# Performance work log

Hardware: AMD Instinct MI355X
Metric: run time of the kernel (lower is better)

## Reference

```python
import jax, jax.numpy as jnp
from jax import lax
import numpy as np

TOP_K = 2
CAPACITY_FACTOR = 1.0


def setup_inputs() -> dict:
    key = jax.random.key(0)
    kx, kg, k1, k2 = jax.random.split(key, 4)
    B, S, D, F, E = 8, 4096, 512, 1024, 16
    x = jax.random.normal(kx, (B, S, D), dtype=jnp.float32)
    w_gate = jax.random.normal(kg, (D, E), dtype=jnp.float32) * 0.02
    w1 = jax.random.normal(k1, (E, D, 2 * F), dtype=jnp.float32) * 0.02
    w2 = jax.random.normal(k2, (E, F, D), dtype=jnp.float32) * 0.02
    return {"x": x, "w_gate": w_gate, "w1": w1, "w2": w2}


def reference(x, w_gate, w1, w2):
    # Inference mode: no gating noise, dropout is identity.
    B, S, D = x.shape
    E = w_gate.shape[1]
    T = B * S
    capacity = max(1, int(CAPACITY_FACTOR * T / E))  # static

    flat = x.reshape(T, D)
    gate_logits = flat @ w_gate                      # [T, E]
    gate_scores = jax.nn.softmax(gate_logits, axis=-1)
    topk_vals, topk_idx = lax.top_k(gate_scores, TOP_K)  # [T, k]

    phi_mean = gate_scores.mean(axis=0)
    aux_loss = E * jnp.sum(phi_mean * phi_mean)

    # Per-expert combine weight for every token: [E, T]
    onehot = topk_idx[None, :, :] == jnp.arange(E)[:, None, None]  # [E, T, k]
    w_et = jnp.sum(jnp.where(onehot, topk_vals[None], 0.0), axis=-1)  # [E, T]

    # Capacity truncation: keep the `capacity` highest-weight tokens per expert
    sel_w, sel_idx = lax.top_k(w_et, capacity)  # [E, C]; unrouted picks have weight 0

    xs = flat[sel_idx]                                  # [E, C, D] gather
    h = jnp.einsum('ecd,edf->ecf', xs, w1)              # [E, C, 2F]
    h1, h2 = jnp.split(h, 2, axis=-1)
    act = h1 * jax.nn.silu(h2)                          # SwiGLU
    out_e = jnp.einsum('ecf,efd->ecd', act, w2) * sel_w[..., None]  # [E, C, D]

    combined = jnp.zeros((T, D), dtype=flat.dtype).at[sel_idx.reshape(-1)].add(
        out_e.reshape(-1, D))
    return combined.reshape(B, S, D), aux_loss
```

## Files before the change

kernel.cpp:

```cpp
#include <hip/hip_runtime.h>
#include <hip/hip_bf16.h>
#include <math.h>

#define T_TOK 32768
#define D_DIM 512
#define E_EXP 16
#define F_DIM 1024
#define C_CAP 2048

typedef __attribute__((ext_vector_type(8))) __bf16 bf16x8;
typedef __attribute__((ext_vector_type(4))) float f32x4;

__device__ __forceinline__ unsigned short f2bf(float f) {
  unsigned u = __float_as_uint(f);
  u += 0x7FFFu + ((u >> 16) & 1u);
  return (unsigned short)(u >> 16);
}

__device__ __forceinline__ void gld16(const void* gptr, void* ldsptr) {
  __builtin_amdgcn_global_load_lds(
      (__attribute__((address_space(1))) void*)(void*)gptr,
      (__attribute__((address_space(3))) void*)ldsptr, 16, 0, 0);
}

__global__ void transpose_conv_kernel(const float* __restrict__ in,
                                      unsigned short* __restrict__ out,
                                      int R, int Cc) {
  __shared__ float tile[32][33];
  int e = blockIdx.z;
  int r0 = blockIdx.y * 32, c0 = blockIdx.x * 32;
  const float* pin = in + (size_t)e * R * Cc;
  unsigned short* pout = out + (size_t)e * R * Cc;
  int tx = threadIdx.x, ty = threadIdx.y;
  #pragma unroll
  for (int i = 0; i < 32; i += 8)
    tile[ty + i][tx] = pin[(size_t)(r0 + ty + i) * Cc + c0 + tx];
  __syncthreads();
  #pragma unroll
  for (int i = 0; i < 32; i += 8)
    pout[(size_t)(c0 + ty + i) * R + r0 + tx] = f2bf(tile[tx][ty + i]);
}

__global__ __launch_bounds__(256) void gate_kernel(
    const float* __restrict__ x, const float* __restrict__ wg,
    float* __restrict__ w_et, float* __restrict__ phi_sum,
    unsigned short* __restrict__ xb) {
  __shared__ float wgl[D_DIM * E_EXP];
  __shared__ float phil[E_EXP];
  int tid = threadIdx.x;
  for (int i = tid; i < D_DIM * E_EXP; i += 256) wgl[i] = wg[i];
  if (tid < E_EXP) phil[tid] = 0.f;
  __syncthreads();

  int g = tid >> 4;
  int e = tid & 15;
  int t = blockIdx.x * 16 + g;

  float acc = 0.f;
  const float* xr = x + (size_t)t * D_DIM;
  #pragma unroll 4
  for (int d = 0; d < D_DIM; d += 4) {
    float4 xv = *(const float4*)(xr + d);
    acc = fmaf(xv.x, wgl[(d + 0) * 16 + e], acc);
    acc = fmaf(xv.y, wgl[(d + 1) * 16 + e], acc);
    acc = fmaf(xv.z, wgl[(d + 2) * 16 + e], acc);
    acc = fmaf(xv.w, wgl[(d + 3) * 16 + e], acc);
  }

  unsigned short* xrow = xb + (size_t)t * D_DIM;
  #pragma unroll
  for (int j = 0; j < 8; ++j) {
    int idx = j * 16 + e;
    float4 v = *(const float4*)(xr + idx * 4);
    ushort4 o;
    o.x = f2bf(v.x); o.y = f2bf(v.y); o.z = f2bf(v.z); o.w = f2bf(v.w);
    ((ushort4*)xrow)[idx] = o;
  }

  float m = acc;
  for (int off = 8; off; off >>= 1) m = fmaxf(m, __shfl_xor(m, off));
  float p = expf(acc - m);
  float s = p;
  for (int off = 8; off; off >>= 1) s += __shfl_xor(s, off);
  float score = p / s;
  atomicAdd(&phil[e], score);

  float v1 = score; int i1 = e;
  for (int off = 8; off; off >>= 1) {
    float ov = __shfl_xor(v1, off); int oi = __shfl_xor(i1, off);
    if (ov > v1 || (ov == v1 && oi < i1)) { v1 = ov; i1 = oi; }
  }
  float sc2 = (e == i1) ? -1.f : score;
  float v2 = sc2; int i2 = e;
  for (int off = 8; off; off >>= 1) {
    float ov = __shfl_xor(v2, off); int oi = __shfl_xor(i2, off);
    if (ov > v2 || (ov == v2 && oi < i2)) { v2 = ov; i2 = oi; }
  }
  if (e == 0) {
    w_et[(size_t)i1 * T_TOK + t] = v1;
    w_et[(size_t)i2 * T_TOK + t] = v2;
  }
  __syncthreads();
  if (tid < E_EXP) atomicAdd(&phi_sum[tid], phil[tid]);
}

__global__ void aux_kernel(const float* __restrict__ phi_sum, float* __restrict__ out_aux) {
  if (threadIdx.x == 0) {
    float s = 0.f;
    for (int e = 0; e < E_EXP; ++e) {
      float pm = phi_sum[e] / (float)T_TOK;
      s += pm * pm;
    }
    *out_aux = (float)E_EXP * s;
  }
}

template<int P>
__global__ __launch_bounds__(256) void s_hist(
    const float* __restrict__ w_et, unsigned* __restrict__ hist,
    const unsigned* __restrict__ prefix, const unsigned* __restrict__ done) {
  int c = blockIdx.x, e = blockIdx.y, tid = threadIdx.x;
  if (P > 0 && done[e]) return;
  __shared__ unsigned lh[2048];
  for (int i = tid; i < 2048; i += 256) lh[i] = 0;
  __syncthreads();
  const float* w = w_et + (size_t)e * T_TOK + c * 2048;
  unsigned pfx = (P > 0) ? prefix[e] : 0u;
  #pragma unroll
  for (int i = 0; i < 8; ++i) {
    unsigned b = __float_as_uint(w[i * 256 + tid]);
    if (P == 0) { if (b) atomicAdd(&lh[b >> 21], 1u); }
    else if (P == 1) { if ((b >> 21) == (pfx >> 21)) atomicAdd(&lh[(b >> 10) & 0x7FFu], 1u); }
    else { if ((b >> 10) == (pfx >> 10)) atomicAdd(&lh[b & 0x3FFu], 1u); }
  }
  __syncthreads();
  for (int i = tid; i < 2048; i += 256)
    if (lh[i]) atomicAdd(&hist[e * 2048 + i], lh[i]);
}

template<int P>
__global__ __launch_bounds__(1024) void s_pick(
    const unsigned* __restrict__ hist, unsigned* __restrict__ prefix,
    unsigned* __restrict__ krem, unsigned* __restrict__ done) {
  int tid = threadIdx.x, lane = tid & 63, e = tid >> 6;
  if (P > 0 && done[e]) return;
  const int BPL = (P == 2) ? 16 : 32;
  const int SH = (P == 0) ? 21 : (P == 1) ? 10 : 0;
  const unsigned* h = hist + e * 2048;
  unsigned S = 0;
  for (int i = 0; i < BPL; ++i) S += h[lane * BPL + i];
  unsigned U = S;
  #pragma unroll
  for (int off = 1; off < 64; off <<= 1) {
    unsigned t = __shfl_down(U, off);
    if (lane + off < 64) U += t;
  }
  unsigned Unext = __shfl_down(U, 1);
  if (lane == 63) Unext = 0;
  unsigned k = (P == 0) ? (unsigned)C_CAP : krem[e];
  if (P == 0 && lane == 0) {
    if (U < k) { done[e] = 1; prefix[e] = 0; krem[e] = 0; }
    else done[e] = 0;
  }
  if (U >= k && Unext < k) {
    unsigned cum = Unext; int chosen = 0; unsigned knew = 0;
    for (int i = BPL - 1; i >= 0; --i) {
      unsigned hh = h[lane * BPL + i];
      if (cum + hh >= k) { chosen = lane * BPL + i; knew = k - cum; break; }
      cum += hh;
    }
    if (P == 0) prefix[e] = ((unsigned)chosen) << SH;
    else prefix[e] = prefix[e] | (((unsigned)chosen) << SH);
    krem[e] = knew;
  }
}

__global__ __launch_bounds__(256) void s_count(
    const float* __restrict__ w_et, const unsigned* __restrict__ prefix,
    unsigned* __restrict__ cnt) {
  int c = blockIdx.x, e = blockIdx.y, tid = threadIdx.x;
  unsigned thr = prefix[e];
  const uint4* up = (const uint4*)(w_et + (size_t)e * T_TOK + c * 2048 + tid * 8);
  uint4 va = up[0], vb = up[1];
  unsigned gt = 0, eq = 0;
  unsigned vals[8] = {va.x, va.y, va.z, va.w, vb.x, vb.y, vb.z, vb.w};
  #pragma unroll
  for (int i = 0; i < 8; ++i) {
    if (vals[i] > thr) gt++;
    else if (vals[i] == thr) eq++;
  }
  __shared__ unsigned sc[256];
  sc[tid] = (gt << 16) | eq;
  __syncthreads();
  for (int s = 128; s; s >>= 1) {
    if (tid < s) sc[tid] += sc[tid + s];
    __syncthreads();
  }
  if (tid == 0) cnt[e * 16 + c] = sc[0];
}

__global__ __launch_bounds__(256) void s_write(
    const float* __restrict__ w_et, const unsigned* __restrict__ prefix,
    const unsigned* __restrict__ cnt,
    int* __restrict__ sel_idx, float* __restrict__ sel_w) {
  int c = blockIdx.x, e = blockIdx.y, tid = threadIdx.x;
  unsigned thr = prefix[e];
  __shared__ unsigned s_gb, s_eb, s_gt, s_eq;
  if (tid == 0) {
    unsigned g = 0, q = 0, gb = 0, eb = 0;
    #pragma unroll
    for (int c2 = 0; c2 < 16; ++c2) {
      unsigned p = cnt[e * 16 + c2];
      if (c2 < c) { gb += p >> 16; eb += p & 0xFFFFu; }
      g += p >> 16; q += p & 0xFFFFu;
    }
    s_gb = gb; s_eb = eb; s_gt = g; s_eq = (unsigned)C_CAP - g;
  }
  const uint4* up = (const uint4*)(w_et + (size_t)e * T_TOK + c * 2048 + tid * 8);
  uint4 va = up[0], vb = up[1];
  unsigned vals[8] = {va.x, va.y, va.z, va.w, vb.x, vb.y, vb.z, vb.w};
  unsigned gt = 0, eq = 0;
  #pragma unroll
  for (int i = 0; i < 8; ++i) {
    if (vals[i] > thr) gt++;
    else if (vals[i] == thr) eq++;
  }
  __shared__ unsigned sc[256];
  unsigned mine = (gt << 16) | eq;
  sc[tid] = mine;
  __syncthreads();
  for (int off = 1; off < 256; off <<= 1) {
    unsigned add = (tid >= off) ? sc[tid - off] : 0u;
    __syncthreads();
    sc[tid] += add;
    __syncthreads();
  }
  unsigned excl = sc[tid] - mine;
  unsigned gpos = s_gb + (excl >> 16);
  unsigned qpos = s_eb + (excl & 0xFFFFu);
  unsigned gtotal = s_gt, eqtake = s_eq;
  int* si = sel_idx + (size_t)e * C_CAP;
  float* sw = sel_w + (size_t)e * C_CAP;
  int tokbase = c * 2048 + tid * 8;
  #pragma unroll
  for (int i = 0; i < 8; ++i) {
    unsigned b = vals[i];
    if (b > thr) {
      si[gpos] = tokbase + i; sw[gpos] = __uint_as_float(b); gpos++;
    } else if (b == thr && qpos < eqtake) {
      si[gtotal + qpos] = tokbase + i; sw[gtotal + qpos] = __uint_as_float(b); qpos++;
    }
  }
}


#define PIPE_BARRIER() do { __builtin_amdgcn_s_barrier(); __builtin_amdgcn_sched_barrier(0); } while (0)

__global__ __launch_bounds__(256, 2) void gemm1_kernel(
    const unsigned short* __restrict__ xb,
    const unsigned short* __restrict__ w1t,
    const int* __restrict__ sel_idx,
    unsigned short* __restrict__ act) {
  __shared__ __align__(16) unsigned short As[5 * 4096];
  __shared__ __align__(16) unsigned short Bs[5 * 4096];
  int bid = (blockIdx.x & 7) * 512 + (blockIdx.x >> 3);
  int nt = bid & 15, mt = (bid >> 4) & 15, e = bid >> 8;
  int tid = threadIdx.x, lane = tid & 63, wid = tid >> 6;
  int wr = wid >> 1, wc = wid & 1;
  int cl = lane & 15, rg = lane >> 4;

  int c0 = tid, c1 = 256 + tid;
  int r0 = c0 >> 2, gk0 = (c0 & 3) ^ ((r0 >> 1) & 3);
  int r1 = c1 >> 2, gk1 = (c1 & 3) ^ ((r1 >> 1) & 3);
  int tok0 = sel_idx[e * C_CAP + mt * 128 + r0];
  int tok1 = sel_idx[e * C_CAP + mt * 128 + r1];
  const unsigned short* ag0 = xb + (size_t)tok0 * D_DIM + gk0 * 8;
  const unsigned short* ag1 = xb + (size_t)tok1 * D_DIM + gk1 * 8;
  int hcol0 = (r0 < 64) ? (nt * 64 + r0) : (F_DIM + nt * 64 + (r0 - 64));
  int hcol1 = (r1 < 64) ? (nt * 64 + r1) : (F_DIM + nt * 64 + (r1 - 64));
  const unsigned short* bg0 = w1t + ((size_t)e * 2 * F_DIM + hcol0) * D_DIM + gk0 * 8;
  const unsigned short* bg1 = w1t + ((size_t)e * 2 * F_DIM + hcol1) * D_DIM + gk1 * 8;
  char* Ab = (char*)As;
  char* Bb = (char*)Bs;

#define G1_STAGE(buf, kt) do { \
    gld16(ag0 + (kt) * 32, Ab + (buf) * 8192 + tid * 16); \
    gld16(ag1 + (kt) * 32, Ab + (buf) * 8192 + 4096 + tid * 16); \
    gld16(bg0 + (kt) * 32, Bb + (buf) * 8192 + tid * 16); \
    gld16(bg1 + (kt) * 32, Bb + (buf) * 8192 + 4096 + tid * 16); \
  } while (0)

  f32x4 zero = {0.f, 0.f, 0.f, 0.f};
  f32x4 acc[4][4];
  #pragma unroll
  for (int m = 0; m < 4; ++m)
    #pragma unroll
    for (int n = 0; n < 4; ++n) acc[m][n] = zero;

#define G1_COMPUTE(buf) do { \
    const unsigned short* Ap = As + (buf) * 4096; \
    const unsigned short* Bp = Bs + (buf) * 4096; \
    bf16x8 av[4], bv[4]; \
    _Pragma("unroll") \
    for (int m = 0; m < 4; ++m) { \
      int ra = wr * 64 + m * 16 + cl; \
      av[m] = *(const bf16x8*)&Ap[(ra * 4 + (rg ^ ((ra >> 1) & 3))) * 8]; \
    } \
    _Pragma("unroll") \
    for (int n = 0; n < 4; ++n) { \
      int rb = ((n < 2) ? (wc * 32 + n * 16) : (64 + wc * 32 + (n - 2) * 16)) + cl; \
      bv[n] = *(const bf16x8*)&Bp[(rb * 4 + (rg ^ ((rb >> 1) & 3))) * 8]; \
    } \
    __builtin_amdgcn_s_setprio(1); \
    _Pragma("unroll") \
    for (int m = 0; m < 4; ++m) \
      _Pragma("unroll") \
      for (int n = 0; n < 4; ++n) \
        acc[m][n] = __builtin_amdgcn_mfma_f32_16x16x32_bf16(av[m], bv[n], acc[m][n], 0, 0, 0); \
    __builtin_amdgcn_s_setprio(0); \
  } while (0)

  const int NK = D_DIM / 32;
  G1_STAGE(0, 0); G1_STAGE(1, 1); G1_STAGE(2, 2); G1_STAGE(3, 3);
  int bc = 0, bs = 4;
  for (int kt = 0; kt < NK - 4; ++kt) {
    asm volatile("s_waitcnt vmcnt(12)" ::: "memory");
    PIPE_BARRIER();
    G1_STAGE(bs, kt + 4);
    bs = (bs == 4) ? 0 : bs + 1;
    __builtin_amdgcn_sched_barrier(0);
    G1_COMPUTE(bc);
    bc = (bc == 4) ? 0 : bc + 1;
  }
  asm volatile("s_waitcnt vmcnt(12)" ::: "memory");
  PIPE_BARRIER();
  G1_COMPUTE(bc); bc = (bc == 4) ? 0 : bc + 1;
  asm volatile("s_waitcnt vmcnt(8)" ::: "memory");
  PIPE_BARRIER();
  G1_COMPUTE(bc); bc = (bc == 4) ? 0 : bc + 1;
  asm volatile("s_waitcnt vmcnt(4)" ::: "memory");
  PIPE_BARRIER();
  G1_COMPUTE(bc); bc = (bc == 4) ? 0 : bc + 1;
  asm volatile("s_waitcnt vmcnt(0)" ::: "memory");
  PIPE_BARRIER();
  G1_COMPUTE(bc);

  #pragma unroll
  for (int m = 0; m < 4; ++m) {
    #pragma unroll
    for (int n = 0; n < 2; ++n) {
      #pragma unroll
      for (int r = 0; r < 4; ++r) {
        int row = mt * 128 + wr * 64 + m * 16 + rg * 4 + r;
        int col = nt * 64 + wc * 32 + n * 16 + cl;
        float h1 = acc[m][n][r];
        float h2 = acc[m][n + 2][r];
        float sg = h2 / (1.f + __expf(-h2));
        act[((size_t)e * C_CAP + row) * F_DIM + col] = f2bf(h1 * sg);
      }
    }
  }
#undef G1_STAGE
#undef G1_COMPUTE
}

__global__ __launch_bounds__(256, 2) void gemm2_kernel(
    const unsigned short* __restrict__ act,
    const unsigned short* __restrict__ w2t,
    const int* __restrict__ sel_idx,
    const float* __restrict__ sel_w,
    float* __restrict__ out) {
  __shared__ __align__(16) unsigned short As[5 * 4096];
  __shared__ __align__(16) unsigned short Bs[5 * 4096];
  int bid = (blockIdx.x & 7) * 128 + (blockIdx.x >> 3);
  int nt = bid & 3, mt = (bid >> 2) & 15, e = bid >> 6;
  int tid = threadIdx.x, lane = tid & 63, wid = tid >> 6;
  int wr = wid >> 1, wc = wid & 1;
  int cl = lane & 15, rg = lane >> 4;

  int c0 = tid, c1 = 256 + tid;
  int r0 = c0 >> 2, gk0 = (c0 & 3) ^ ((r0 >> 1) & 3);
  int r1 = c1 >> 2, gk1 = (c1 & 3) ^ ((r1 >> 1) & 3);
  const unsigned short* ag0 = act + ((size_t)e * C_CAP + mt * 128 + r0) * F_DIM + gk0 * 8;
  const unsigned short* ag1 = act + ((size_t)e * C_CAP + mt * 128 + r1) * F_DIM + gk1 * 8;
  const unsigned short* bg0 = w2t + ((size_t)e * D_DIM + nt * 128 + r0) * F_DIM + gk0 * 8;
  const unsigned short* bg1 = w2t + ((size_t)e * D_DIM + nt * 128 + r1) * F_DIM + gk1 * 8;
  char* Ab = (char*)As;
  char* Bb = (char*)Bs;

#define G2_STAGE(buf, kt) do { \
    gld16(ag0 + (kt) * 32, Ab + (buf) * 8192 + tid * 16); \
    gld16(ag1 + (kt) * 32, Ab + (buf) * 8192 + 4096 + tid * 16); \
    gld16(bg0 + (kt) * 32, Bb + (buf) * 8192 + tid * 16); \
    gld16(bg1 + (kt) * 32, Bb + (buf) * 8192 + 4096 + tid * 16); \
  } while (0)

  f32x4 zero = {0.f, 0.f, 0.f, 0.f};
  f32x4 acc[4][4];
  #pragma unroll
  for (int m = 0; m < 4; ++m)
    #pragma unroll
    for (int n = 0; n < 4; ++n) acc[m][n] = zero;

#define G2_COMPUTE(buf) do { \
    const unsigned short* Ap = As + (buf) * 4096; \
    const unsigned short* Bp = Bs + (buf) * 4096; \
    bf16x8 av[4], bv[4]; \
    _Pragma("unroll") \
    for (int m = 0; m < 4; ++m) { \
      int ra = wr * 64 + m * 16 + cl; \
      av[m] = *(const bf16x8*)&Ap[(ra * 4 + (rg ^ ((ra >> 1) & 3))) * 8]; \
    } \
    _Pragma("unroll") \
    for (int n = 0; n < 4; ++n) { \
      int rb = wc * 64 + n * 16 + cl; \
      bv[n] = *(const bf16x8*)&Bp[(rb * 4 + (rg ^ ((rb >> 1) & 3))) * 8]; \
    } \
    __builtin_amdgcn_s_setprio(1); \
    _Pragma("unroll") \
    for (int m = 0; m < 4; ++m) \
      _Pragma("unroll") \
      for (int n = 0; n < 4; ++n) \
        acc[m][n] = __builtin_amdgcn_mfma_f32_16x16x32_bf16(av[m], bv[n], acc[m][n], 0, 0, 0); \
    __builtin_amdgcn_s_setprio(0); \
  } while (0)

  const int NK = F_DIM / 32;
  G2_STAGE(0, 0); G2_STAGE(1, 1); G2_STAGE(2, 2); G2_STAGE(3, 3);
  int bc = 0, bs = 4;
  for (int kt = 0; kt < NK - 4; ++kt) {
    asm volatile("s_waitcnt vmcnt(12)" ::: "memory");
    PIPE_BARRIER();
    G2_STAGE(bs, kt + 4);
    bs = (bs == 4) ? 0 : bs + 1;
    __builtin_amdgcn_sched_barrier(0);
    G2_COMPUTE(bc);
    bc = (bc == 4) ? 0 : bc + 1;
  }
  asm volatile("s_waitcnt vmcnt(12)" ::: "memory");
  PIPE_BARRIER();
  G2_COMPUTE(bc); bc = (bc == 4) ? 0 : bc + 1;
  asm volatile("s_waitcnt vmcnt(8)" ::: "memory");
  PIPE_BARRIER();
  G2_COMPUTE(bc); bc = (bc == 4) ? 0 : bc + 1;
  asm volatile("s_waitcnt vmcnt(4)" ::: "memory");
  PIPE_BARRIER();
  G2_COMPUTE(bc); bc = (bc == 4) ? 0 : bc + 1;
  asm volatile("s_waitcnt vmcnt(0)" ::: "memory");
  PIPE_BARRIER();
  G2_COMPUTE(bc);

  #pragma unroll
  for (int m = 0; m < 4; ++m) {
    #pragma unroll
    for (int r = 0; r < 4; ++r) {
      int slot = mt * 128 + wr * 64 + m * 16 + rg * 4 + r;
      float wgt = sel_w[e * C_CAP + slot];
      int tok = sel_idx[e * C_CAP + slot];
      float* orow = out + (size_t)tok * D_DIM;
      #pragma unroll
      for (int n = 0; n < 4; ++n) {
        int col = nt * 128 + wc * 64 + n * 16 + cl;
        atomicAdd(&orow[col], acc[m][n][r] * wgt);
      }
    }
  }
#undef G2_STAGE
#undef G2_COMPUTE
}

extern "C" void kernel_launch(void* const* d_in, const int* in_sizes, int n_in,
                              void* d_out, int out_size, void* d_ws, size_t ws_size,
                              hipStream_t stream) {
  const float* x  = (const float*)d_in[0];
  const float* wg = (const float*)d_in[1];
  const float* w1 = (const float*)d_in[2];
  const float* w2 = (const float*)d_in[3];
  float* out = (float*)d_out;

  char* ws = (char*)d_ws;
  size_t off = 0;
  auto carve = [&](size_t bytes) -> void* {
    void* p = ws + off;
    off += (bytes + 255) & ~(size_t)255;
    return p;
  };
  float* w_et            = (float*)carve((size_t)E_EXP * T_TOK * 4);
  float* phi             = (float*)carve(64);
  int* sel_i             = (int*)carve((size_t)E_EXP * C_CAP * 4);
  float* sel_wv          = (float*)carve((size_t)E_EXP * C_CAP * 4);
  unsigned short* xb     = (unsigned short*)carve((size_t)T_TOK * D_DIM * 2);
  unsigned short* w1t    = (unsigned short*)carve((size_t)E_EXP * 2 * F_DIM * D_DIM * 2);
  unsigned short* w2t    = (unsigned short*)carve((size_t)E_EXP * D_DIM * F_DIM * 2);
  unsigned short* actb   = (unsigned short*)carve((size_t)E_EXP * C_CAP * F_DIM * 2);
  unsigned* hist0        = (unsigned*)carve((size_t)E_EXP * 2048 * 4);
  unsigned* hist1        = (unsigned*)carve((size_t)E_EXP * 2048 * 4);
  unsigned* hist2        = (unsigned*)carve((size_t)E_EXP * 2048 * 4);
  unsigned* prefix       = (unsigned*)carve(64 * 4);
  unsigned* krem         = (unsigned*)carve(64 * 4);
  unsigned* done         = (unsigned*)carve(64 * 4);
  unsigned* cnt          = (unsigned*)carve(256 * 4);
  if (off > ws_size) return;

  hipMemsetAsync(w_et, 0, (size_t)E_EXP * T_TOK * 4, stream);
  hipMemsetAsync(phi, 0, 64, stream);
  hipMemsetAsync(hist0, 0, (size_t)E_EXP * 2048 * 4 * 3, stream);
  hipMemsetAsync(d_out, 0, (size_t)out_size * 4, stream);

  transpose_conv_kernel<<<dim3(2 * F_DIM / 32, D_DIM / 32, E_EXP), dim3(32, 8), 0, stream>>>(
      w1, w1t, D_DIM, 2 * F_DIM);
  transpose_conv_kernel<<<dim3(D_DIM / 32, F_DIM / 32, E_EXP), dim3(32, 8), 0, stream>>>(
      w2, w2t, F_DIM, D_DIM);
  gate_kernel<<<T_TOK / 16, 256, 0, stream>>>(x, wg, w_et, phi, xb);

  s_hist<0><<<dim3(16, 16), 256, 0, stream>>>(w_et, hist0, prefix, done);
  s_pick<0><<<1, 1024, 0, stream>>>(hist0, prefix, krem, done);
  s_hist<1><<<dim3(16, 16), 256, 0, stream>>>(w_et, hist1, prefix, done);
  s_pick<1><<<1, 1024, 0, stream>>>(hist1, prefix, krem, done);
  s_hist<2><<<dim3(16, 16), 256, 0, stream>>>(w_et, hist2, prefix, done);
  s_pick<2><<<1, 1024, 0, stream>>>(hist2, prefix, krem, done);
  s_count<<<dim3(16, 16), 256, 0, stream>>>(w_et, prefix, cnt);
  s_write<<<dim3(16, 16), 256, 0, stream>>>(w_et, prefix, cnt, sel_i, sel_wv);

  aux_kernel<<<1, 64, 0, stream>>>(phi, out + (size_t)T_TOK * D_DIM);
  gemm1_kernel<<<E_EXP * 16 * 16, 256, 0, stream>>>(xb, w1t, sel_i, actb);
  gemm2_kernel<<<E_EXP * 16 * 4, 256, 0, stream>>>(actb, w2t, sel_i, sel_wv, out);
}
```

Measured before the change: 341.6 us.

## Widen GEMM N-tiles, shorten pipeline, fuse radix-select pick into histogram

Both expert GEMMs move from 128x128 tiles to 128x256 tiles, with 8 MFMA accumulators per row and a 3-stage instead of a 5-stage LDS pipeline. This raises operand reuse per block and halves the grid, but increases register pressure and leaves fewer blocks. The separate s_pick kernels are folded into s_hist using an arrival counter, so the last block per expert does the pick and three launches go away. The transpose kernel now writes vectorized ushort4 stores.

```diff
diff --git a/kernel.cpp b/kernel.cpp
--- a/kernel.cpp
+++ b/kernel.cpp
@@ -36,9 +36,14 @@
   for (int i = 0; i < 32; i += 8)
     tile[ty + i][tx] = pin[(size_t)(r0 + ty + i) * Cc + c0 + tx];
   __syncthreads();
-  #pragma unroll
-  for (int i = 0; i < 32; i += 8)
-    pout[(size_t)(c0 + ty + i) * R + r0 + tx] = f2bf(tile[tx][ty + i]);
+  int t = ty * 32 + tx;
+  int oc = t >> 3, og = t & 7;
+  ushort4 o;
+  o.x = f2bf(tile[og * 4 + 0][oc]);
+  o.y = f2bf(tile[og * 4 + 1][oc]);
+  o.z = f2bf(tile[og * 4 + 2][oc]);
+  o.w = f2bf(tile[og * 4 + 3][oc]);
+  *(ushort4*)&pout[(size_t)(c0 + oc) * R + r0 + og * 4] = o;
 }
 
 __global__ __launch_bounds__(256) void gate_kernel(
@@ -118,7 +123,8 @@
 template<int P>
 __global__ __launch_bounds__(256) void s_hist(
     const float* __restrict__ w_et, unsigned* __restrict__ hist,
-    const unsigned* __restrict__ prefix, const unsigned* __restrict__ done) {
+    unsigned* __restrict__ prefix, unsigned* __restrict__ krem,
+    unsigned* __restrict__ done, unsigned* __restrict__ arrive) {
   int c = blockIdx.x, e = blockIdx.y, tid = threadIdx.x;
   if (P > 0 && done[e]) return;
   __shared__ unsigned lh[2048];
@@ -136,14 +142,15 @@
   __syncthreads();
   for (int i = tid; i < 2048; i += 256)
     if (lh[i]) atomicAdd(&hist[e * 2048 + i], lh[i]);
-}
-
-template<int P>
-__global__ __launch_bounds__(1024) void s_pick(
-    const unsigned* __restrict__ hist, unsigned* __restrict__ prefix,
-    unsigned* __restrict__ krem, unsigned* __restrict__ done) {
-  int tid = threadIdx.x, lane = tid & 63, e = tid >> 6;
-  if (P > 0 && done[e]) return;
+
+  __threadfence();
+  __shared__ unsigned s_last;
+  if (tid == 0) s_last = (atomicAdd(&arrive[P * 16 + e], 1u) == 15u) ? 1u : 0u;
+  __syncthreads();
+  if (!s_last) return;
+  __threadfence();
+  if (tid >= 64) return;
+  int lane = tid;
   const int BPL = (P == 2) ? 16 : 32;
   const int SH = (P == 0) ? 21 : (P == 1) ? 10 : 0;
   const unsigned* h = hist + e * 2048;
@@ -152,8 +159,8 @@
   unsigned U = S;
   #pragma unroll
   for (int off = 1; off < 64; off <<= 1) {
-    unsigned t = __shfl_down(U, off);
-    if (lane + off < 64) U += t;
+    unsigned t2 = __shfl_down(U, off);
+    if (lane + off < 64) U += t2;
   }
   unsigned Unext = __shfl_down(U, 1);
   if (lane == 63) Unext = 0;
@@ -261,86 +268,88 @@
     const unsigned short* __restrict__ w1t,
     const int* __restrict__ sel_idx,
     unsigned short* __restrict__ act) {
-  __shared__ __align__(16) unsigned short As[5 * 4096];
-  __shared__ __align__(16) unsigned short Bs[5 * 4096];
-  int bid = (blockIdx.x & 7) * 512 + (blockIdx.x >> 3);
-  int nt = bid & 15, mt = (bid >> 4) & 15, e = bid >> 8;
+  __shared__ __align__(16) unsigned short As[3 * 4096];
+  __shared__ __align__(16) unsigned short Bs[3 * 8192];
+  int bid = (blockIdx.x & 7) * 256 + (blockIdx.x >> 3);
+  int nt = bid & 7, mt = (bid >> 3) & 15, e = bid >> 7;
   int tid = threadIdx.x, lane = tid & 63, wid = tid >> 6;
   int wr = wid >> 1, wc = wid & 1;
   int cl = lane & 15, rg = lane >> 4;
 
-  int c0 = tid, c1 = 256 + tid;
-  int r0 = c0 >> 2, gk0 = (c0 & 3) ^ ((r0 >> 1) & 3);
-  int r1 = c1 >> 2, gk1 = (c1 & 3) ^ ((r1 >> 1) & 3);
-  int tok0 = sel_idx[e * C_CAP + mt * 128 + r0];
-  int tok1 = sel_idx[e * C_CAP + mt * 128 + r1];
-  const unsigned short* ag0 = xb + (size_t)tok0 * D_DIM + gk0 * 8;
-  const unsigned short* ag1 = xb + (size_t)tok1 * D_DIM + gk1 * 8;
-  int hcol0 = (r0 < 64) ? (nt * 64 + r0) : (F_DIM + nt * 64 + (r0 - 64));
-  int hcol1 = (r1 < 64) ? (nt * 64 + r1) : (F_DIM + nt * 64 + (r1 - 64));
-  const unsigned short* bg0 = w1t + ((size_t)e * 2 * F_DIM + hcol0) * D_DIM + gk0 * 8;
-  const unsigned short* bg1 = w1t + ((size_t)e * 2 * F_DIM + hcol1) * D_DIM + gk1 * 8;
+  const unsigned short* agA[2];
+  const unsigned short* bgB[4];
+  #pragma unroll
+  for (int s = 0; s < 2; ++s) {
+    int c = s * 256 + tid;
+    int row = c >> 2, j = c & 3;
+    int gk = j ^ ((row >> 1) & 3);
+    int tok = sel_idx[e * C_CAP + mt * 128 + row];
+    agA[s] = xb + (size_t)tok * D_DIM + gk * 8;
+  }
+  #pragma unroll
+  for (int s = 0; s < 4; ++s) {
+    int c = s * 256 + tid;
+    int rb = c >> 2, j = c & 3;
+    int gk = j ^ ((rb >> 1) & 3);
+    int t = rb & 127, w2 = rb >> 7;
+    int hcol = (t < 64) ? (nt * 128 + w2 * 64 + t)
+                        : (F_DIM + nt * 128 + w2 * 64 + (t - 64));
+    bgB[s] = w1t + ((size_t)e * 2 * F_DIM + hcol) * D_DIM + gk * 8;
+  }
   char* Ab = (char*)As;
   char* Bb = (char*)Bs;
 
 #define G1_STAGE(buf, kt) do { \
-    gld16(ag0 + (kt) * 32, Ab + (buf) * 8192 + tid * 16); \
-    gld16(ag1 + (kt) * 32, Ab + (buf) * 8192 + 4096 + tid * 16); \
-    gld16(bg0 + (kt) * 32, Bb + (buf) * 8192 + tid * 16); \
-    gld16(bg1 + (kt) * 32, Bb + (buf) * 8192 + 4096 + tid * 16); \
+    gld16(agA[0] + (kt) * 32, Ab + (buf) * 8192 + tid * 16); \
+    gld16(agA[1] + (kt) * 32, Ab + (buf) * 8192 + 4096 + tid * 16); \
+    gld16(bgB[0] + (kt) * 32, Bb + (buf) * 16384 + tid * 16); \
+    gld16(bgB[1] + (kt) * 32, Bb + (buf) * 16384 + 4096 + tid * 16); \
+    gld16(bgB[2] + (kt) * 32, Bb + (buf) * 16384 + 8192 + tid * 16); \
+    gld16(bgB[3] + (kt) * 32, Bb + (buf) * 16384 + 12288 + tid * 16); \
   } while (0)
 
   f32x4 zero = {0.f, 0.f, 0.f, 0.f};
-  f32x4 acc[4][4];
+  f32x4 acc[4][8];
   #pragma unroll
   for (int m = 0; m < 4; ++m)
     #pragma unroll
-    for (int n = 0; n < 4; ++n) acc[m][n] = zero;
+    for (int n = 0; n < 8; ++n) acc[m][n] = zero;
 
 #define G1_COMPUTE(buf) do { \
     const unsigned short* Ap = As + (buf) * 4096; \
-    const unsigned short* Bp = Bs + (buf) * 4096; \
-    bf16x8 av[4], bv[4]; \
+    const unsigned short* Bp = Bs + (buf) * 8192; \
+    bf16x8 av[4], bv[8]; \
     _Pragma("unroll") \
     for (int m = 0; m < 4; ++m) { \
       int ra = wr * 64 + m * 16 + cl; \
       av[m] = *(const bf16x8*)&Ap[(ra * 4 + (rg ^ ((ra >> 1) & 3))) * 8]; \
     } \
     _Pragma("unroll") \
-    for (int n = 0; n < 4; ++n) { \
-      int rb = ((n < 2) ? (wc * 32 + n * 16) : (64 + wc * 32 + (n - 2) * 16)) + cl; \
+    for (int n = 0; n < 8; ++n) { \
+      int rb = wc * 128 + n * 16 + cl; \
       bv[n] = *(const bf16x8*)&Bp[(rb * 4 + (rg ^ ((rb >> 1) & 3))) * 8]; \
     } \
     __builtin_amdgcn_s_setprio(1); \
     _Pragma("unroll") \
     for (int m = 0; m < 4; ++m) \
       _Pragma("unroll") \
-      for (int n = 0; n < 4; ++n) \
+      for (int n = 0; n < 8; ++n) \
         acc[m][n] = __builtin_amdgcn_mfma_f32_16x16x32_bf16(av[m], bv[n], acc[m][n], 0, 0, 0); \
     __builtin_amdgcn_s_setprio(0); \
   } while (0)
 
   const int NK = D_DIM / 32;
-  G1_STAGE(0, 0); G1_STAGE(1, 1); G1_STAGE(2, 2); G1_STAGE(3, 3);
-  int bc = 0, bs = 4;
-  for (int kt = 0; kt < NK - 4; ++kt) {
-    asm volatile("s_waitcnt vmcnt(12)" ::: "memory");
+  G1_STAGE(0, 0);
+  G1_STAGE(1, 1);
+  int bc = 0, bs = 2;
+  for (int kt = 0; kt < NK - 1; ++kt) {
+    asm volatile("s_waitcnt vmcnt(6)" ::: "memory");
     PIPE_BARRIER();
-    G1_STAGE(bs, kt + 4);
-    bs = (bs == 4) ? 0 : bs + 1;
+    if (kt + 2 < NK) { G1_STAGE(bs, kt + 2); bs = (bs == 2) ? 0 : bs + 1; }
     __builtin_amdgcn_sched_barrier(0);
     G1_COMPUTE(bc);
-    bc = (bc == 4) ? 0 : bc + 1;
-  }
-  asm volatile("s_waitcnt vmcnt(12)" ::: "memory");
-  PIPE_BARRIER();
-  G1_COMPUTE(bc); bc = (bc == 4) ? 0 : bc + 1;
-  asm volatile("s_waitcnt vmcnt(8)" ::: "memory");
-  PIPE_BARRIER();
-  G1_COMPUTE(bc); bc = (bc == 4) ? 0 : bc + 1;
-  asm volatile("s_waitcnt vmcnt(4)" ::: "memory");
-  PIPE_BARRIER();
-  G1_COMPUTE(bc); bc = (bc == 4) ? 0 : bc + 1;
+    bc = (bc == 2) ? 0 : bc + 1;
+  }
   asm volatile("s_waitcnt vmcnt(0)" ::: "memory");
   PIPE_BARRIER();
   G1_COMPUTE(bc);
@@ -348,13 +357,13 @@
   #pragma unroll
   for (int m = 0; m < 4; ++m) {
     #pragma unroll
-    for (int n = 0; n < 2; ++n) {
+    for (int n = 0; n < 4; ++n) {
       #pragma unroll
       for (int r = 0; r < 4; ++r) {
         int row = mt * 128 + wr * 64 + m * 16 + rg * 4 + r;
-        int col = nt * 64 + wc * 32 + n * 16 + cl;
+        int col = nt * 128 + wc * 64 + n * 16 + cl;
         float h1 = acc[m][n][r];
-        float h2 = acc[m][n + 2][r];
+        float h2 = acc[m][n + 4][r];
         float sg = h2 / (1.f + __expf(-h2));
         act[((size_t)e * C_CAP + row) * F_DIM + col] = f2bf(h1 * sg);
       }
@@ -370,82 +379,85 @@
     const int* __restrict__ sel_idx,
     const float* __restrict__ sel_w,
     float* __restrict__ out) {
-  __shared__ __align__(16) unsigned short As[5 * 4096];
-  __shared__ __align__(16) unsigned short Bs[5 * 4096];
-  int bid = (blockIdx.x & 7) * 128 + (blockIdx.x >> 3);
-  int nt = bid & 3, mt = (bid >> 2) & 15, e = bid >> 6;
+  __shared__ __align__(16) unsigned short As[3 * 4096];
+  __shared__ __align__(16) unsigned short Bs[3 * 8192];
+  int bid = (blockIdx.x & 7) * 64 + (blockIdx.x >> 3);
+  int nt = bid & 1, mt = (bid >> 1) & 15, e = bid >> 5;
   int tid = threadIdx.x, lane = tid & 63, wid = tid >> 6;
   int wr = wid >> 1, wc = wid & 1;
   int cl = lane & 15, rg = lane >> 4;
 
-  int c0 = tid, c1 = 256 + tid;
-  int r0 = c0 >> 2, gk0 = (c0 & 3) ^ ((r0 >> 1) & 3);
-  int r1 = c1 >> 2, gk1 = (c1 & 3) ^ ((r1 >> 1) & 3);
-  const unsigned short* ag0 = act + ((size_t)e * C_CAP + mt * 128 + r0) * F_DIM + gk0 * 8;
-  const unsigned short* ag1 = act + ((size_t)e * C_CAP + mt * 128 + r1) * F_DIM + gk1 * 8;
-  const unsigned short* bg0 = w2t + ((size_t)e * D_DIM + nt * 128 + r0) * F_DIM + gk0 * 8;
-  const unsigned short* bg1 = w2t + ((size_t)e * D_DIM + nt * 128 + r1) * F_DIM + gk1 * 8;
+  const unsigned short* agA[2];
+  const unsigned short* bgB[4];
+  #pragma unroll
+  for (int s = 0; s < 2; ++s) {
+    int c = s * 256 + tid;
+    int row = c >> 2, j = c & 3;
+    int gk = j ^ ((row >> 1) & 3);
+    agA[s] = act + ((size_t)e * C_CAP + mt * 128 + row) * F_DIM + gk * 8;
+  }
+  #pragma unroll
+  for (int s = 0; s < 4; ++s) {
+    int c = s * 256 + tid;
+    int rb = c >> 2, j = c & 3;
+    int gk = j ^ ((rb >> 1) & 3);
+    int dcol = nt * 256 + rb;
+    bgB[s] = w2t + ((size_t)e * D_DIM + dcol) * F_DIM + gk * 8;
+  }
   char* Ab = (char*)As;
   char* Bb = (char*)Bs;
 
 #define G2_STAGE(buf, kt) do { \
-    gld16(ag0 + (kt) * 32, Ab + (buf) * 8192 + tid * 16); \
-    gld16(ag1 + (kt) * 32, Ab + (buf) * 8192 + 4096 + tid * 16); \
-    gld16(bg0 + (kt) * 32, Bb + (buf) * 8192 + tid * 16); \
-    gld16(bg1 + (kt) * 32, Bb + (buf) * 8192 + 4096 + tid * 16); \
+    gld16(agA[0] + (kt) * 32, Ab + (buf) * 8192 + tid * 16); \
+    gld16(agA[1] + (kt) * 32, Ab + (buf) * 8192 + 4096 + tid * 16); \
+    gld16(bgB[0] + (kt) * 32, Bb + (buf) * 16384 + tid * 16); \
+    gld16(bgB[1] + (kt) * 32, Bb + (buf) * 16384 + 4096 + tid * 16); \
+    gld16(bgB[2] + (kt) * 32, Bb + (buf) * 16384 + 8192 + tid * 16); \
+    gld16(bgB[3] + (kt) * 32, Bb + (buf) * 16384 + 12288 + tid * 16); \
   } while (0)
 
   f32x4 zero = {0.f, 0.f, 0.f, 0.f};
-  f32x4 acc[4][4];
+  f32x4 acc[4][8];
   #pragma unroll
   for (int m = 0; m < 4; ++m)
     #pragma unroll
-    for (int n = 0; n < 4; ++n) acc[m][n] = zero;
+    for (int n = 0; n < 8; ++n) acc[m][n] = zero;
 
 #define G2_COMPUTE(buf) do { \
     const unsigned short* Ap = As + (buf) * 4096; \
-    const unsigned short* Bp = Bs + (buf) * 4096; \
-    bf16x8 av[4], bv[4]; \
+    const unsigned short* Bp = Bs + (buf) * 8192; \
+    bf16x8 av[4], bv[8]; \
     _Pragma("unroll") \
     for (int m = 0; m < 4; ++m) { \
       int ra = wr * 64 + m * 16 + cl; \
       av[m] = *(const bf16x8*)&Ap[(ra * 4 + (rg ^ ((ra >> 1) & 3))) * 8]; \
     } \
     _Pragma("unroll") \
-    for (int n = 0; n < 4; ++n) { \
-      int rb = wc * 64 + n * 16 + cl; \
+    for (int n = 0; n < 8; ++n) { \
+      int rb = wc * 128 + n * 16 + cl; \
       bv[n] = *(const bf16x8*)&Bp[(rb * 4 + (rg ^ ((rb >> 1) & 3))) * 8]; \
     } \
     __builtin_amdgcn_s_setprio(1); \
     _Pragma("unroll") \
     for (int m = 0; m < 4; ++m) \
       _Pragma("unroll") \
-      for (int n = 0; n < 4; ++n) \
+      for (int n = 0; n < 8; ++n) \
         acc[m][n] = __builtin_amdgcn_mfma_f32_16x16x32_bf16(av[m], bv[n], acc[m][n], 0, 0, 0); \
     __builtin_amdgcn_s_setprio(0); \
   } while (0)
 
   const int NK = F_DIM / 32;
-  G2_STAGE(0, 0); G2_STAGE(1, 1); G2_STAGE(2, 2); G2_STAGE(3, 3);
-  int bc = 0, bs = 4;
-  for (int kt = 0; kt < NK - 4; ++kt) {
-    asm volatile("s_waitcnt vmcnt(12)" ::: "memory");
+  G2_STAGE(0, 0);
+  G2_STAGE(1, 1);
+  int bc = 0, bs = 2;
+  for (int kt = 0; kt < NK - 1; ++kt) {
+    asm volatile("s_waitcnt vmcnt(6)" ::: "memory");
     PIPE_BARRIER();
-    G2_STAGE(bs, kt + 4);
-    bs = (bs == 4) ? 0 : bs + 1;
+    if (kt + 2 < NK) { G2_STAGE(bs, kt + 2); bs = (bs == 2) ? 0 : bs + 1; }
     __builtin_amdgcn_sched_barrier(0);
     G2_COMPUTE(bc);
-    bc = (bc == 4) ? 0 : bc + 1;
-  }
-  asm volatile("s_waitcnt vmcnt(12)" ::: "memory");
-  PIPE_BARRIER();
-  G2_COMPUTE(bc); bc = (bc == 4) ? 0 : bc + 1;
-  asm volatile("s_waitcnt vmcnt(8)" ::: "memory");
-  PIPE_BARRIER();
-  G2_COMPUTE(bc); bc = (bc == 4) ? 0 : bc + 1;
-  asm volatile("s_waitcnt vmcnt(4)" ::: "memory");
-  PIPE_BARRIER();
-  G2_COMPUTE(bc); bc = (bc == 4) ? 0 : bc + 1;
+    bc = (bc == 2) ? 0 : bc + 1;
+  }
   asm volatile("s_waitcnt vmcnt(0)" ::: "memory");
   PIPE_BARRIER();
   G2_COMPUTE(bc);
@@ -459,8 +471,8 @@
       int tok = sel_idx[e * C_CAP + slot];
       float* orow = out + (size_t)tok * D_DIM;
       #pragma unroll
-      for (int n = 0; n < 4; ++n) {
-        int col = nt * 128 + wc * 64 + n * 16 + cl;
+      for (int n = 0; n < 8; ++n) {
+        int col = nt * 256 + wc * 128 + n * 16 + cl;
         atomicAdd(&orow[col], acc[m][n][r] * wgt);
       }
     }
@@ -500,11 +512,13 @@
   unsigned* krem         = (unsigned*)carve(64 * 4);
   unsigned* done         = (unsigned*)carve(64 * 4);
   unsigned* cnt          = (unsigned*)carve(256 * 4);
+  unsigned* arrive       = (unsigned*)carve(64 * 4);
   if (off > ws_size) return;
 
   hipMemsetAsync(w_et, 0, (size_t)E_EXP * T_TOK * 4, stream);
   hipMemsetAsync(phi, 0, 64, stream);
   hipMemsetAsync(hist0, 0, (size_t)E_EXP * 2048 * 4 * 3, stream);
+  hipMemsetAsync(arrive, 0, 64 * 4, stream);
   hipMemsetAsync(d_out, 0, (size_t)out_size * 4, stream);
 
   transpose_conv_kernel<<<dim3(2 * F_DIM / 32, D_DIM / 32, E_EXP), dim3(32, 8), 0, stream>>>(
@@ -513,16 +527,13 @@
       w2, w2t, F_DIM, D_DIM);
   gate_kernel<<<T_TOK / 16, 256, 0, stream>>>(x, wg, w_et, phi, xb);
 
-  s_hist<0><<<dim3(16, 16), 256, 0, stream>>>(w_et, hist0, prefix, done);
-  s_pick<0><<<1, 1024, 0, stream>>>(hist0, prefix, krem, done);
-  s_hist<1><<<dim3(16, 16), 256, 0, stream>>>(w_et, hist1, prefix, done);
-  s_pick<1><<<1, 1024, 0, stream>>>(hist1, prefix, krem, done);
-  s_hist<2><<<dim3(16, 16), 256, 0, stream>>>(w_et, hist2, prefix, done);
-  s_pick<2><<<1, 1024, 0, stream>>>(hist2, prefix, krem, done);
+  s_hist<0><<<dim3(16, 16), 256, 0, stream>>>(w_et, hist0, prefix, krem, done, arrive);
+  s_hist<1><<<dim3(16, 16), 256, 0, stream>>>(w_et, hist1, prefix, krem, done, arrive);
+  s_hist<2><<<dim3(16, 16), 256, 0, stream>>>(w_et, hist2, prefix, krem, done, arrive);
   s_count<<<dim3(16, 16), 256, 0, stream>>>(w_et, prefix, cnt);
   s_write<<<dim3(16, 16), 256, 0, stream>>>(w_et, prefix, cnt, sel_i, sel_wv);
 
   aux_kernel<<<1, 64, 0, stream>>>(phi, out + (size_t)T_TOK * D_DIM);
-  gemm1_kernel<<<E_EXP * 16 * 16, 256, 0, stream>>>(xb, w1t, sel_i, actb);
-  gemm2_kernel<<<E_EXP * 16 * 4, 256, 0, stream>>>(actb, w2t, sel_i, sel_wv, out);
-}
+  gemm1_kernel<<<E_EXP * 16 * 8, 256, 0, stream>>>(xb, w1t, sel_i, actb);
+  gemm2_kernel<<<E_EXP * 16 * 2, 256, 0, stream>>>(actb, w2t, sel_i, sel_wv, out);
+}
```

New measurement: 366.4 us. +7.3%, slower.
